# Kernel tuning notes

Measured on AMD Instinct MI355X. Metric: run time of the kernel, lower is better.

The kernel has to match this reference:

```python
import jax, jax.numpy as jnp
import numpy as np

N, E, F = 20000, 160000, 128
H, C1, C2 = 4, 128, 256
G, NCLS = 64, 10


def setup_inputs() -> dict:
    key = jax.random.key(0)
    ks = jax.random.split(key, 14)
    s = 0.05
    inp = {
        "x": jax.random.normal(ks[0], (N, F), jnp.float32),
        "edge_index": jax.random.randint(ks[1], (2, E), 0, N, dtype=jnp.int32),
        "batch": ((jnp.arange(N, dtype=jnp.int32) * G) // N),  # sorted graph ids, all 64 graphs non-empty
        # GATConv 1: in=128 -> 128 per head, heads=4, concat -> 512
        "W1": jax.random.normal(ks[2], (F, H * C1), jnp.float32) * s,
        "att_src1": jax.random.normal(ks[3], (H, C1), jnp.float32) * s,
        "att_dst1": jax.random.normal(ks[4], (H, C1), jnp.float32) * s,
        "b1": jnp.zeros((H * C1,), jnp.float32),
        # GATConv 2: in=512 -> 256, heads=1, concat=False
        "W2": jax.random.normal(ks[5], (H * C1, C2), jnp.float32) * s,
        "att_src2": jax.random.normal(ks[6], (1, C2), jnp.float32) * s,
        "att_dst2": jax.random.normal(ks[7], (1, C2), jnp.float32) * s,
        "b2": jnp.zeros((C2,), jnp.float32),
        # fc head
        "fc1_w": jax.random.normal(ks[8], (C2, 64), jnp.float32) * s,
        "fc1_b": jnp.zeros((64,), jnp.float32),
        "fc2_w": jax.random.normal(ks[9], (64, NCLS), jnp.float32) * s,
        "fc2_b": jnp.zeros((NCLS,), jnp.float32),
    }
    return inp


def gat_conv(x, src, dst, W, att_src, att_dst, bias, concat):
    """PyG GATConv: per-edge attention + segment softmax over dst + scatter-add."""
    n = x.shape[0]
    h_, c_ = att_src.shape
    h = (x @ W).reshape(n, h_, c_)                    # [N,H,C]
    a_src = jnp.einsum('nhc,hc->nh', h, att_src)       # [N,H]
    a_dst = jnp.einsum('nhc,hc->nh', h, att_dst)       # [N,H]
    e = jax.nn.leaky_relu(a_src[src] + a_dst[dst], negative_slope=0.2)  # [Etot,H]
    e_max = jax.ops.segment_max(e, dst, num_segments=n)
    ee = jnp.exp(e - e_max[dst])
    denom = jax.ops.segment_sum(ee, dst, num_segments=n)
    alpha = ee / denom[dst]                            # [Etot,H]
    out = jax.ops.segment_sum(h[src] * alpha[:, :, None], dst, num_segments=n)  # [N,H,C]
    out = out.reshape(n, h_ * c_) if concat else out.mean(axis=1)
    return out + bias


def reference(x, edge_index, batch, W1, att_src1, att_dst1, b1,
              W2, att_src2, att_dst2, b2, fc1_w, fc1_b, fc2_w, fc2_b):
    n = x.shape[0]
    # to_undirected: both directions; plus self-loops (GATConv add_self_loops=True)
    loops = jnp.arange(n, dtype=edge_index.dtype)
    src = jnp.concatenate([edge_index[0], edge_index[1], loops])
    dst = jnp.concatenate([edge_index[1], edge_index[0], loops])
    h = gat_conv(x, src, dst, W1, att_src1, att_dst1, b1, concat=True)
    h = jax.nn.relu(h)
    h = gat_conv(h, src, dst, W2, att_src2, att_dst2, b2, concat=False)
    g = jax.ops.segment_max(h, batch, num_segments=G)  # global_max_pool
    g = jax.nn.relu(g @ fc1_w + fc1_b) @ fc2_w + fc2_b
    return jax.nn.log_softmax(g, axis=1)
```

## Files before the change

### kernel.cpp

```cpp
#include <hip/hip_runtime.h>
#include <math.h>

#define FDIM 128
#define HEADS 4
#define C1DIM 128
#define C2DIM 256
#define NGRAPH 64
#define NCLS 10
#define DEGCAP 64
#define LOG2E 1.44269504088896340736f

typedef __attribute__((ext_vector_type(8))) short short8;
typedef __attribute__((ext_vector_type(4))) float float4v;
typedef __attribute__((ext_vector_type(2))) float floatx2;

__device__ __forceinline__ unsigned short f2bf(float f) {
    unsigned u = __builtin_bit_cast(unsigned, f);
    unsigned r = (u + 0x7FFFu + ((u >> 16) & 1u)) >> 16;
    return (unsigned short)r;
}
__device__ __forceinline__ float lrelu(float x) { return x > 0.f ? x : 0.2f * x; }
__device__ __forceinline__ float sel4(float a, float b, float c, float d, int hd) {
    return hd == 0 ? a : hd == 1 ? b : hd == 2 ? c : d;
}
__device__ __forceinline__ float wexp2(float x) { return __builtin_amdgcn_exp2f(lrelu(x)); }
__device__ __forceinline__ unsigned char f2fp8(float f) {
    return (unsigned char)(__builtin_amdgcn_cvt_pk_fp8_f32(f, f, 0, false) & 0xff);
}
__device__ __forceinline__ void fp8x8_dec2(int2 r, floatx2* p) {
    p[0] = __builtin_amdgcn_cvt_pk_f32_fp8(r.x, false);
    p[1] = __builtin_amdgcn_cvt_pk_f32_fp8(r.x, true);
    p[2] = __builtin_amdgcn_cvt_pk_f32_fp8(r.y, false);
    p[3] = __builtin_amdgcn_cvt_pk_f32_fp8(r.y, true);
}
__device__ __forceinline__ void fp8x4_dec2(int r, floatx2* p) {
    p[0] = __builtin_amdgcn_cvt_pk_f32_fp8(r, false);
    p[1] = __builtin_amdgcn_cvt_pk_f32_fp8(r, true);
}
__device__ __forceinline__ unsigned encf(float v) {
    unsigned b = __builtin_bit_cast(unsigned, v);
    return (b & 0x80000000u) ? ~b : (b | 0x80000000u);
}
__device__ __forceinline__ float decf(unsigned u) {
    unsigned b = (u & 0x80000000u) ? (u ^ 0x80000000u) : ~u;
    return __builtin_bit_cast(float, b);
}

__global__ __launch_bounds__(256) void prep_kernel(
        int* __restrict__ zero_base, int nzero_words,
        const float* __restrict__ x, unsigned short* __restrict__ xb, int n4,
        const float* __restrict__ W1, unsigned short* __restrict__ W1t,
        const float* __restrict__ W2, unsigned short* __restrict__ W2t,
        int ZB, int CB) {
    __shared__ float tile[32][33];
    int blk = blockIdx.x;
    if (blk < ZB) {
        int i = blk * 256 + threadIdx.x;
        if (i < nzero_words) zero_base[i] = 0;
        return;
    }
    blk -= ZB;
    if (blk < CB) {
        int i = blk * 256 + threadIdx.x;
        if (i < n4) {
            float4 v = ((const float4*)x)[i];
            ushort4 o;
            o.x = f2bf(v.x); o.y = f2bf(v.y); o.z = f2bf(v.z); o.w = f2bf(v.w);
            ((ushort4*)xb)[i] = o;
        }
        return;
    }
    blk -= CB;
    const float* W; unsigned short* Wt; int K, Nc, bx, by;
    if (blk < 64) {
        W = W1; Wt = W1t; K = 128; Nc = 512;
        bx = (blk & 15) * 32; by = (blk >> 4) * 32;
    } else {
        blk -= 64;
        W = W2; Wt = W2t; K = 512; Nc = 256;
        bx = (blk & 7) * 32; by = (blk >> 3) * 32;
    }
    int tx = threadIdx.x & 31, ty = threadIdx.x >> 5;
    #pragma unroll
    for (int r = 0; r < 32; r += 8)
        tile[ty + r][tx] = W[(size_t)(by + ty + r) * Nc + bx + tx];
    __syncthreads();
    #pragma unroll
    for (int r = 0; r < 32; r += 8)
        Wt[(size_t)(bx + ty + r) * K + by + tx] = f2bf(tile[tx][ty + r]);
}

template<int MODE>
__global__ __launch_bounds__(256) void bgemm_kernel(
        const unsigned short* __restrict__ A,
        const unsigned short* __restrict__ Bt,
        unsigned char* __restrict__ Cout,
        const float* __restrict__ att_src,
        const float* __restrict__ att_dst,
        float* __restrict__ as_out,
        float* __restrict__ ad_out,
        int M, int N_, int K,
        const int* __restrict__ ei, int E,
        int* __restrict__ cnt, int* __restrict__ esrc, int SB) {
    if (MODE == 1 && blockIdx.x < SB) {
        int i = blockIdx.x * 256 + threadIdx.x;
        if (i < 2 * E) {
            int src = ei[i];
            int dst = (i < E) ? ei[E + i] : ei[i - E];
            int pos = atomicAdd(&cnt[dst], 1);
            if (pos < DEGCAP) esrc[(dst << 6) + pos] = src;
        }
        return;
    }
    constexpr int BN = (MODE == 1) ? 128 : 256;
    constexpr int JW = BN / 32;
    constexpr int CPADB = BN + 16;
    constexpr int SMEMB = 4096 + BN * 64;
    __shared__ __align__(16) unsigned char smem[SMEMB];
    unsigned short* As = (unsigned short*)smem;
    unsigned short* Bs = (unsigned short*)(smem + 4096);
    __shared__ float sd_s[4][32];
    __shared__ float sd_d[4][32];
    const int t = threadIdx.x;
    const int lane = t & 63;
    const int wave = t >> 6;
    int row0, col0, headi;
    if (MODE == 1) {
        int bb = blockIdx.x - SB;
        headi = bb & 3;
        col0 = headi * BN;
        row0 = (bb >> 2) * 64;
    } else {
        headi = 0;
        col0 = 0;
        row0 = blockIdx.x * 64;
    }
    const int wr = (wave >> 1) * 32, wc = (wave & 1) * (BN / 2);
    float4v acc[2][JW] = {};
    for (int k0 = 0; k0 < K; k0 += 32) {
        {
            int i = t;
            int gr = row0 + (i >> 2); if (gr >= M) gr = M - 1;
            const unsigned short* gp = A + (size_t)gr * K + k0 + ((i & 3) << 3);
            __builtin_amdgcn_global_load_lds(
                (const __attribute__((address_space(1))) unsigned int*)gp,
                (__attribute__((address_space(3))) unsigned int*)&As[i * 8], 16, 0, 0);
        }
        #pragma unroll
        for (int c = 0; c < BN / 64; ++c) {
            int i = c * 256 + t;
            int gn = col0 + (i >> 2);
            const unsigned short* gp = Bt + (size_t)gn * K + k0 + ((i & 3) << 3);
            __builtin_amdgcn_global_load_lds(
                (const __attribute__((address_space(1))) unsigned int*)gp,
                (__attribute__((address_space(3))) unsigned int*)&Bs[i * 8], 16, 0, 0);
        }
        __syncthreads();
        short8 af[2], bfr[JW];
        #pragma unroll
        for (int i = 0; i < 2; ++i)
            af[i] = *(const short8*)&As[(wr + i * 16 + (lane & 15)) * 32 + (lane >> 4) * 8];
        #pragma unroll
        for (int j = 0; j < JW; ++j)
            bfr[j] = *(const short8*)&Bs[(wc + j * 16 + (lane & 15)) * 32 + (lane >> 4) * 8];
        #pragma unroll
        for (int i = 0; i < 2; ++i)
            #pragma unroll
            for (int j = 0; j < JW; ++j)
                acc[i][j] = __builtin_amdgcn_mfma_f32_16x16x32_bf16(af[i], bfr[j], acc[i][j], 0, 0, 0);
        __syncthreads();
    }
    float asv[JW], adv[JW];
    #pragma unroll
    for (int j = 0; j < JW; ++j) {
        int cc = col0 + wc + j * 16 + (lane & 15);
        asv[j] = att_src[cc];
        adv[j] = att_dst[cc];
    }
    #pragma unroll
    for (int i = 0; i < 2; ++i) {
        #pragma unroll
        for (int p = 0; p < 4; ++p) {
            int rr = wr + i * 16 + (lane >> 4) * 4 + p;
            float s = 0.f, d = 0.f;
            #pragma unroll
            for (int j = 0; j < JW; ++j) {
                smem[rr * CPADB + wc + j * 16 + (lane & 15)] = f2fp8(acc[i][j][p]);
                s += acc[i][j][p] * asv[j];
                d += acc[i][j][p] * adv[j];
            }
            #pragma unroll
            for (int o = 1; o <= 8; o <<= 1) { s += __shfl_xor(s, o); d += __shfl_xor(d, o); }
            if ((lane & 15) == 0) {
                int ridx = i * 16 + (lane >> 4) * 4 + p;
                sd_s[wave][ridx] = s;
                sd_d[wave][ridx] = d;
            }
        }
    }
    __syncthreads();
    #pragma unroll
    for (int it = 0; it < BN / 64; ++it) {
        int idx = it * 256 + t;
        int row = idx / (BN / 16), c16 = (idx % (BN / 16)) * 16;
        int grw = row0 + row;
        if (grw < M)
            *(int4*)&Cout[(size_t)grw * N_ + col0 + c16] = *(const int4*)&smem[row * CPADB + c16];
    }
    if ((wave & 1) == 0 && lane < 32) {
        float s = (sd_s[wave][lane] + sd_s[wave + 1][lane]) * LOG2E;
        float d = (sd_d[wave][lane] + sd_d[wave + 1][lane]) * LOG2E;
        int r = row0 + wr + lane;
        if (r < M) {
            if (MODE == 1) {
                as_out[r * 4 + headi] = s;
                ad_out[r * 4 + headi] = d;
            } else {
                as_out[r] = s;
                ad_out[r] = d;
            }
        }
    }
}

__global__ __launch_bounds__(256) void edge_agg1_kernel(
        const unsigned char* __restrict__ h1f8,
        const float4* __restrict__ as14,
        const float4* __restrict__ ad14,
        const int* __restrict__ cnt,
        const int* __restrict__ esrc,
        const float* __restrict__ b1,
        unsigned short* __restrict__ ho1b, int N) {
    __shared__ int sl_s[4][64];
    __shared__ __align__(16) float4 w_s[4][64];
    int wave = threadIdx.x >> 6, lane = threadIdx.x & 63;
    int node = blockIdx.x * 4 + wave;
    if (node >= N) return;
    int deg = cnt[node]; if (deg > DEGCAP) deg = DEGCAP;
    int ebase = node << 6;
    float4 asn = as14[node], adn = ad14[node];
    float w0 = wexp2(asn.x + adn.x);
    float w1 = wexp2(asn.y + adn.y);
    float w2 = wexp2(asn.z + adn.z);
    float w3 = wexp2(asn.w + adn.w);
    int hd = lane >> 4;
    unsigned c0 = (unsigned)lane * 8;
    float wsh = sel4(w0, w1, w2, w3, hd);
    floatx2 acc2[4];
    {
        int2 rs = *(const int2*)(h1f8 + ((unsigned)node << 9) + c0);
        floatx2 ds[4]; fp8x8_dec2(rs, ds);
        #pragma unroll
        for (int k = 0; k < 4; ++k) acc2[k] = wsh * ds[k];
    }
    float d0 = 0.f, d1 = 0.f, d2 = 0.f, d3 = 0.f;
    for (int cb = 0; cb < deg; cb += 64) {
        int idx = cb + lane;
        int sl = esrc[ebase + (idx < deg ? idx : deg - 1)];
        float4 wl = make_float4(0.f, 0.f, 0.f, 0.f);
        if (idx < deg) {
            float4 a = as14[sl];
            wl.x = wexp2(a.x + adn.x);
            wl.y = wexp2(a.y + adn.y);
            wl.z = wexp2(a.z + adn.z);
            wl.w = wexp2(a.w + adn.w);
            d0 += wl.x; d1 += wl.y; d2 += wl.z; d3 += wl.w;
        }
        sl_s[wave][lane] = sl << 9;
        w_s[wave][lane] = wl;
        int jmax = deg - cb; if (jmax > 64) jmax = 64;
        int j = 0;
        for (; j + 8 <= jmax; j += 8) {
            unsigned o[8]; float u[8];
            #pragma unroll
            for (int q = 0; q < 8; ++q) {
                o[q] = (unsigned)sl_s[wave][j + q] + c0;
                u[q] = ((const float*)&w_s[wave][j + q])[hd];
            }
            int2 r[8];
            #pragma unroll
            for (int q = 0; q < 8; ++q) r[q] = *(const int2*)(h1f8 + o[q]);
            #pragma unroll
            for (int q = 0; q < 8; ++q) {
                floatx2 f[4]; fp8x8_dec2(r[q], f);
                #pragma unroll
                for (int k = 0; k < 4; ++k) acc2[k] += u[q] * f[k];
            }
        }
        for (; j < jmax; ++j) {
            unsigned o0 = (unsigned)sl_s[wave][j] + c0;
            float u = ((const float*)&w_s[wave][j])[hd];
            int2 r = *(const int2*)(h1f8 + o0);
            floatx2 f[4]; fp8x8_dec2(r, f);
            #pragma unroll
            for (int k = 0; k < 4; ++k) acc2[k] += u * f[k];
        }
    }
    #pragma unroll
    for (int o = 32; o > 0; o >>= 1) {
        d0 += __shfl_xor(d0, o); d1 += __shfl_xor(d1, o);
        d2 += __shfl_xor(d2, o); d3 += __shfl_xor(d3, o);
    }
    d0 += w0; d1 += w1; d2 += w2; d3 += w3;
    float dh = sel4(d0, d1, d2, d3, hd);
    float inv = 1.f / dh;
    float4 bA = *(const float4*)&b1[c0], bB = *(const float4*)&b1[c0 + 4];
    float v0 = fmaxf(acc2[0].x * inv + bA.x, 0.f), v1 = fmaxf(acc2[0].y * inv + bA.y, 0.f);
    float v2 = fmaxf(acc2[1].x * inv + bA.z, 0.f), v3 = fmaxf(acc2[1].y * inv + bA.w, 0.f);
    float v4 = fmaxf(acc2[2].x * inv + bB.x, 0.f), v5 = fmaxf(acc2[2].y * inv + bB.y, 0.f);
    float v6 = fmaxf(acc2[3].x * inv + bB.z, 0.f), v7 = fmaxf(acc2[3].y * inv + bB.w, 0.f);
    int4 o;
    o.x = (int)((unsigned)f2bf(v0) | ((unsigned)f2bf(v1) << 16));
    o.y = (int)((unsigned)f2bf(v2) | ((unsigned)f2bf(v3) << 16));
    o.z = (int)((unsigned)f2bf(v4) | ((unsigned)f2bf(v5) << 16));
    o.w = (int)((unsigned)f2bf(v6) | ((unsigned)f2bf(v7) << 16));
    *(int4*)&ho1b[(size_t)node * 512 + c0] = o;
}

__global__ __launch_bounds__(256) void edge_agg2_kernel(
        const unsigned char* __restrict__ h2f8,
        const float* __restrict__ as2,
        const float* __restrict__ ad2,
        const int* __restrict__ cnt,
        const int* __restrict__ esrc,
        const float* __restrict__ b2,
        const int* __restrict__ batch,
        unsigned* __restrict__ pool, int N) {
    __shared__ unsigned pms[4][256];
    __shared__ int sl_s[4][64];
    __shared__ float w_s[4][64];
    int wave = threadIdx.x >> 6, lane = threadIdx.x & 63;
    int node = blockIdx.x * 4 + wave;
    bool valid = node < N;
    unsigned c0 = (unsigned)lane * 4;
    unsigned e0 = 0, e1 = 0, e2 = 0, e3 = 0;
    if (valid) {
        int deg = cnt[node]; if (deg > DEGCAP) deg = DEGCAP;
        int ebase = node << 6;
        float adn = ad2[node];
        float wself = wexp2(as2[node] + adn);
        floatx2 acc2[2];
        {
            int r = *(const int*)(h2f8 + ((unsigned)node << 8) + c0);
            floatx2 ds[2]; fp8x4_dec2(r, ds);
            acc2[0] = wself * ds[0];
            acc2[1] = wself * ds[1];
        }
        float dsum = 0.f;
        for (int cb = 0; cb < deg; cb += 64) {
            int idx = cb + lane;
            int sl = esrc[ebase + (idx < deg ? idx : deg - 1)];
            float wl = 0.f;
            if (idx < deg) {
                wl = wexp2(as2[sl] + adn);
                dsum += wl;
            }
            sl_s[wave][lane] = sl << 8;
            w_s[wave][lane] = wl;
            int jmax = deg - cb; if (jmax > 64) jmax = 64;
            int j = 0;
            for (; j + 8 <= jmax; j += 8) {
                unsigned oo[8]; float u[8]; int r[8];
                #pragma unroll
                for (int q = 0; q < 8; ++q) {
                    oo[q] = (unsigned)sl_s[wave][j + q] + c0;
                    u[q] = w_s[wave][j + q];
                }
                #pragma unroll
                for (int q = 0; q < 8; ++q) r[q] = *(const int*)(h2f8 + oo[q]);
                #pragma unroll
                for (int q = 0; q < 8; ++q) {
                    floatx2 f[2]; fp8x4_dec2(r[q], f);
                    acc2[0] += u[q] * f[0];
                    acc2[1] += u[q] * f[1];
                }
            }
            for (; j < jmax; ++j) {
                unsigned o0 = (unsigned)sl_s[wave][j] + c0;
                float u = w_s[wave][j];
                int r = *(const int*)(h2f8 + o0);
                floatx2 f[2]; fp8x4_dec2(r, f);
                acc2[0] += u * f[0];
                acc2[1] += u * f[1];
            }
        }
        #pragma unroll
        for (int o = 32; o > 0; o >>= 1) dsum += __shfl_xor(dsum, o);
        dsum += wself;
        float inv = 1.f / dsum;
        float4 bv = *(const float4*)&b2[c0];
        e0 = encf(acc2[0].x * inv + bv.x);
        e1 = encf(acc2[0].y * inv + bv.y);
        e2 = encf(acc2[1].x * inv + bv.z);
        e3 = encf(acc2[1].y * inv + bv.w);
    }
    pms[wave][c0]     = e0;
    pms[wave][c0 + 1] = e1;
    pms[wave][c0 + 2] = e2;
    pms[wave][c0 + 3] = e3;
    __syncthreads();
    int n0 = blockIdx.x * 4;
    int n3 = n0 + 3; if (n3 >= N) n3 = N - 1;
    int g0 = batch[n0], g3 = batch[n3];
    if (g0 == g3) {
        int tt = threadIdx.x;
        unsigned m0 = pms[0][tt] > pms[1][tt] ? pms[0][tt] : pms[1][tt];
        unsigned m1 = pms[2][tt] > pms[3][tt] ? pms[2][tt] : pms[3][tt];
        unsigned m = m0 > m1 ? m0 : m1;
        atomicMax(&pool[(size_t)g0 * 256 + tt], m);
    } else if (valid) {
        int g = batch[node];
        atomicMax(&pool[(size_t)g * 256 + c0], e0);
        atomicMax(&pool[(size_t)g * 256 + c0 + 1], e1);
        atomicMax(&pool[(size_t)g * 256 + c0 + 2], e2);
        atomicMax(&pool[(size_t)g * 256 + c0 + 3], e3);
    }
}

__global__ __launch_bounds__(64) void head_kernel(const unsigned* __restrict__ pool,
                                                  const float* __restrict__ fc1w,
                                                  const float* __restrict__ fc1b,
                                                  const float* __restrict__ fc2w,
                                                  const float* __restrict__ fc2b,
                                                  float* __restrict__ out) {
    __shared__ float gr[256];
    __shared__ float hid[64];
    __shared__ float o10[NCLS];
    int g = blockIdx.x, t = threadIdx.x;
    for (int i = t; i < 256; i += 64)
        gr[i] = decf(pool[(size_t)g * 256 + i]);
    __syncthreads();
    float s = fc1b[t];
    for (int k = 0; k < 256; ++k) s += gr[k] * fc1w[k * 64 + t];
    hid[t] = s > 0.f ? s : 0.f;
    __syncthreads();
    if (t < NCLS) {
        float s2 = fc2b[t];
        for (int k = 0; k < 64; ++k) s2 += hid[k] * fc2w[k * NCLS + t];
        o10[t] = s2;
    }
    __syncthreads();
    if (t == 0) {
        float mx = -INFINITY;
        for (int c = 0; c < NCLS; ++c) mx = fmaxf(mx, o10[c]);
        float se = 0.f;
        for (int c = 0; c < NCLS; ++c) se += __expf(o10[c] - mx);
        float lse = mx + logf(se);
        for (int c = 0; c < NCLS; ++c) out[g * NCLS + c] = o10[c] - lse;
    }
}

extern "C" void kernel_launch(void* const* d_in, const int* in_sizes, int n_in,
                              void* d_out, int out_size, void* d_ws, size_t ws_size,
                              hipStream_t stream) {
    (void)n_in; (void)out_size; (void)ws_size;
    const float* x        = (const float*)d_in[0];
    const int*   ei       = (const int*)d_in[1];
    const int*   batch    = (const int*)d_in[2];
    const float* W1       = (const float*)d_in[3];
    const float* att_src1 = (const float*)d_in[4];
    const float* att_dst1 = (const float*)d_in[5];
    const float* b1       = (const float*)d_in[6];
    const float* W2       = (const float*)d_in[7];
    const float* att_src2 = (const float*)d_in[8];
    const float* att_dst2 = (const float*)d_in[9];
    const float* b2       = (const float*)d_in[10];
    const float* fc1w     = (const float*)d_in[11];
    const float* fc1b     = (const float*)d_in[12];
    const float* fc2w     = (const float*)d_in[13];
    const float* fc2b     = (const float*)d_in[14];

    const int N = in_sizes[2];
    const int E = in_sizes[1] / 2;
    const int tot = 2 * E;

    char* base = (char*)d_ws;
    size_t off = 0;
    auto alloc = [&](size_t bytes) -> void* {
        void* p = base + off;
        off = (off + bytes + 255) & ~(size_t)255;
        return p;
    };
    int*      cnt    = (int*)alloc((size_t)N * 4);
    unsigned* pool   = (unsigned*)alloc((size_t)NGRAPH * 256 * 4);
    size_t zend = off;
    int*   esrc   = (int*)alloc((size_t)N * DEGCAP * 4);
    float* as1    = (float*)alloc((size_t)N * HEADS * 4);
    float* ad1    = (float*)alloc((size_t)N * HEADS * 4);
    float* as2    = (float*)alloc((size_t)N * 4);
    float* ad2    = (float*)alloc((size_t)N * 4);
    unsigned short* xb   = (unsigned short*)alloc((size_t)N * FDIM * 2);
    unsigned short* W1t  = (unsigned short*)alloc((size_t)512 * 128 * 2);
    unsigned short* W2t  = (unsigned short*)alloc((size_t)256 * 512 * 2);
    unsigned char*  h1f8 = (unsigned char*)alloc((size_t)N * 512);
    unsigned short* ho1b = (unsigned short*)alloc((size_t)N * 512 * 2);
    unsigned char*  h2f8 = (unsigned char*)alloc((size_t)N * 256);

    int nzero = (int)((zend - (size_t)((char*)cnt - base)) / 4);
    int ZB = (nzero + 255) / 256;
    int n4 = N * FDIM / 4;
    int CB = (n4 + 255) / 256;
    prep_kernel<<<ZB + CB + 64 + 128, 256, 0, stream>>>(
        cnt, nzero, x, xb, n4, W1, W1t, W2, W2t, ZB, CB);

    int SB = (tot + 255) / 256;
    int rowb = (N + 63) / 64;
    bgemm_kernel<1><<<SB + 4 * rowb, 256, 0, stream>>>(
        xb, W1t, h1f8, att_src1, att_dst1, as1, ad1, N, 512, 128, ei, E, cnt, esrc, SB);

    edge_agg1_kernel<<<(N + 3) / 4, 256, 0, stream>>>(h1f8, (const float4*)as1, (const float4*)ad1,
                                                      cnt, esrc, b1, ho1b, N);

    bgemm_kernel<2><<<rowb, 256, 0, stream>>>(
        ho1b, W2t, h2f8, att_src2, att_dst2, as2, ad2, N, 256, 512,
        nullptr, 0, nullptr, nullptr, 0);

    edge_agg2_kernel<<<(N + 3) / 4, 256, 0, stream>>>(h2f8, as2, ad2, cnt, esrc, b2,
                                                      batch, pool, N);

    head_kernel<<<NGRAPH, 64, 0, stream>>>(pool, fc1w, fc1b, fc2w, fc2b, (float*)d_out);
}
```

Measured before the change: 188.1 us.

## Split each node's edge aggregation across two waves with LDS reduction

Both edge aggregation kernels now assign two waves per destination node. Each wave handles alternate neighbours (even or odd), and the partial accumulators and softmax denominators are combined through shared memory after a block barrier. The goal is to halve the serial gather chain per wave and raise memory-level parallelism for the fp8 neighbour loads. In exchange it doubles the block count, adds barriers and LDS traffic, and leaves half the waves idle during the epilogue. The pooling step now handles pairs of nodes per block.

```diff
diff --git a/kernel.cpp b/kernel.cpp
--- a/kernel.cpp
+++ b/kernel.cpp
@@ -231,46 +231,51 @@
         const int* __restrict__ esrc,
         const float* __restrict__ b1,
         unsigned short* __restrict__ ho1b, int N) {
-    __shared__ int sl_s[4][64];
-    __shared__ __align__(16) float4 w_s[4][64];
+    __shared__ int sl_s[4][32];
+    __shared__ __align__(16) float4 w_s[4][32];
+    __shared__ float dsum_s[2][2][4];
+    __shared__ __align__(16) float accbuf[2][64][8];
     int wave = threadIdx.x >> 6, lane = threadIdx.x & 63;
-    int node = blockIdx.x * 4 + wave;
-    if (node >= N) return;
-    int deg = cnt[node]; if (deg > DEGCAP) deg = DEGCAP;
-    int ebase = node << 6;
-    float4 asn = as14[node], adn = ad14[node];
-    float w0 = wexp2(asn.x + adn.x);
-    float w1 = wexp2(asn.y + adn.y);
-    float w2 = wexp2(asn.z + adn.z);
-    float w3 = wexp2(asn.w + adn.w);
+    int nib = wave >> 1, half = wave & 1;
+    int node = blockIdx.x * 2 + nib;
+    bool valid = node < N;
     int hd = lane >> 4;
     unsigned c0 = (unsigned)lane * 8;
-    float wsh = sel4(w0, w1, w2, w3, hd);
-    floatx2 acc2[4];
-    {
-        int2 rs = *(const int2*)(h1f8 + ((unsigned)node << 9) + c0);
-        floatx2 ds[4]; fp8x8_dec2(rs, ds);
-        #pragma unroll
-        for (int k = 0; k < 4; ++k) acc2[k] = wsh * ds[k];
-    }
+    floatx2 acc2[4] = {};
     float d0 = 0.f, d1 = 0.f, d2 = 0.f, d3 = 0.f;
-    for (int cb = 0; cb < deg; cb += 64) {
-        int idx = cb + lane;
-        int sl = esrc[ebase + (idx < deg ? idx : deg - 1)];
-        float4 wl = make_float4(0.f, 0.f, 0.f, 0.f);
-        if (idx < deg) {
+    float ws0 = 0.f, ws1 = 0.f, ws2 = 0.f, ws3 = 0.f;
+    int nh = 0;
+    if (valid) {
+        int deg = cnt[node]; if (deg > DEGCAP) deg = DEGCAP;
+        int ebase = node << 6;
+        float4 adn = ad14[node];
+        nh = (deg + 1 - half) >> 1;
+        if (lane < nh) {
+            int sl = esrc[ebase + half + 2 * lane];
             float4 a = as14[sl];
+            float4 wl;
             wl.x = wexp2(a.x + adn.x);
             wl.y = wexp2(a.y + adn.y);
             wl.z = wexp2(a.z + adn.z);
             wl.w = wexp2(a.w + adn.w);
-            d0 += wl.x; d1 += wl.y; d2 += wl.z; d3 += wl.w;
-        }
-        sl_s[wave][lane] = sl << 9;
-        w_s[wave][lane] = wl;
-        int jmax = deg - cb; if (jmax > 64) jmax = 64;
+            d0 = wl.x; d1 = wl.y; d2 = wl.z; d3 = wl.w;
+            sl_s[wave][lane] = sl << 9;
+            w_s[wave][lane] = wl;
+        }
+        if (half == 0) {
+            float4 asn = as14[node];
+            ws0 = wexp2(asn.x + adn.x);
+            ws1 = wexp2(asn.y + adn.y);
+            ws2 = wexp2(asn.z + adn.z);
+            ws3 = wexp2(asn.w + adn.w);
+            float wsh = sel4(ws0, ws1, ws2, ws3, hd);
+            int2 rs = *(const int2*)(h1f8 + ((unsigned)node << 9) + c0);
+            floatx2 ds[4]; fp8x8_dec2(rs, ds);
+            #pragma unroll
+            for (int k = 0; k < 4; ++k) acc2[k] = wsh * ds[k];
+        }
         int j = 0;
-        for (; j + 8 <= jmax; j += 8) {
+        for (; j + 8 <= nh; j += 8) {
             unsigned o[8]; float u[8];
             #pragma unroll
             for (int q = 0; q < 8; ++q) {
@@ -287,7 +292,7 @@
                 for (int k = 0; k < 4; ++k) acc2[k] += u[q] * f[k];
             }
         }
-        for (; j < jmax; ++j) {
+        for (; j < nh; ++j) {
             unsigned o0 = (unsigned)sl_s[wave][j] + c0;
             float u = ((const float*)&w_s[wave][j])[hd];
             int2 r = *(const int2*)(h1f8 + o0);
@@ -301,20 +306,35 @@
         d0 += __shfl_xor(d0, o); d1 += __shfl_xor(d1, o);
         d2 += __shfl_xor(d2, o); d3 += __shfl_xor(d3, o);
     }
-    d0 += w0; d1 += w1; d2 += w2; d3 += w3;
-    float dh = sel4(d0, d1, d2, d3, hd);
-    float inv = 1.f / dh;
-    float4 bA = *(const float4*)&b1[c0], bB = *(const float4*)&b1[c0 + 4];
-    float v0 = fmaxf(acc2[0].x * inv + bA.x, 0.f), v1 = fmaxf(acc2[0].y * inv + bA.y, 0.f);
-    float v2 = fmaxf(acc2[1].x * inv + bA.z, 0.f), v3 = fmaxf(acc2[1].y * inv + bA.w, 0.f);
-    float v4 = fmaxf(acc2[2].x * inv + bB.x, 0.f), v5 = fmaxf(acc2[2].y * inv + bB.y, 0.f);
-    float v6 = fmaxf(acc2[3].x * inv + bB.z, 0.f), v7 = fmaxf(acc2[3].y * inv + bB.w, 0.f);
-    int4 o;
-    o.x = (int)((unsigned)f2bf(v0) | ((unsigned)f2bf(v1) << 16));
-    o.y = (int)((unsigned)f2bf(v2) | ((unsigned)f2bf(v3) << 16));
-    o.z = (int)((unsigned)f2bf(v4) | ((unsigned)f2bf(v5) << 16));
-    o.w = (int)((unsigned)f2bf(v6) | ((unsigned)f2bf(v7) << 16));
-    *(int4*)&ho1b[(size_t)node * 512 + c0] = o;
+    if (half == 0) { d0 += ws0; d1 += ws1; d2 += ws2; d3 += ws3; }
+    if (lane == 0) {
+        dsum_s[nib][half][0] = d0; dsum_s[nib][half][1] = d1;
+        dsum_s[nib][half][2] = d2; dsum_s[nib][half][3] = d3;
+    }
+    if (half == 1) {
+        *(float4*)&accbuf[nib][lane][0] = make_float4(acc2[0].x, acc2[0].y, acc2[1].x, acc2[1].y);
+        *(float4*)&accbuf[nib][lane][4] = make_float4(acc2[2].x, acc2[2].y, acc2[3].x, acc2[3].y);
+    }
+    __syncthreads();
+    if (valid && half == 0) {
+        float4 A0 = *(const float4*)&accbuf[nib][lane][0];
+        float4 A1 = *(const float4*)&accbuf[nib][lane][4];
+        acc2[0].x += A0.x; acc2[0].y += A0.y; acc2[1].x += A0.z; acc2[1].y += A0.w;
+        acc2[2].x += A1.x; acc2[2].y += A1.y; acc2[3].x += A1.z; acc2[3].y += A1.w;
+        float dh = dsum_s[nib][0][hd] + dsum_s[nib][1][hd];
+        float inv = 1.f / dh;
+        float4 bA = *(const float4*)&b1[c0], bB = *(const float4*)&b1[c0 + 4];
+        float v0 = fmaxf(acc2[0].x * inv + bA.x, 0.f), v1 = fmaxf(acc2[0].y * inv + bA.y, 0.f);
+        float v2 = fmaxf(acc2[1].x * inv + bA.z, 0.f), v3 = fmaxf(acc2[1].y * inv + bA.w, 0.f);
+        float v4 = fmaxf(acc2[2].x * inv + bB.x, 0.f), v5 = fmaxf(acc2[2].y * inv + bB.y, 0.f);
+        float v6 = fmaxf(acc2[3].x * inv + bB.z, 0.f), v7 = fmaxf(acc2[3].y * inv + bB.w, 0.f);
+        int4 o;
+        o.x = (int)((unsigned)f2bf(v0) | ((unsigned)f2bf(v1) << 16));
+        o.y = (int)((unsigned)f2bf(v2) | ((unsigned)f2bf(v3) << 16));
+        o.z = (int)((unsigned)f2bf(v4) | ((unsigned)f2bf(v5) << 16));
+        o.w = (int)((unsigned)f2bf(v6) | ((unsigned)f2bf(v7) << 16));
+        *(int4*)&ho1b[(size_t)node * 512 + c0] = o;
+    }
 }
 
 __global__ __launch_bounds__(256) void edge_agg2_kernel(
@@ -326,94 +346,100 @@
         const float* __restrict__ b2,
         const int* __restrict__ batch,
         unsigned* __restrict__ pool, int N) {
-    __shared__ unsigned pms[4][256];
-    __shared__ int sl_s[4][64];
-    __shared__ float w_s[4][64];
+    __shared__ unsigned pms[2][256];
+    __shared__ int sl_s[4][32];
+    __shared__ float w_s[4][32];
+    __shared__ float dsum_s[2][2];
+    __shared__ __align__(16) float accbuf[2][64][4];
     int wave = threadIdx.x >> 6, lane = threadIdx.x & 63;
-    int node = blockIdx.x * 4 + wave;
+    int nib = wave >> 1, half = wave & 1;
+    int node = blockIdx.x * 2 + nib;
     bool valid = node < N;
     unsigned c0 = (unsigned)lane * 4;
-    unsigned e0 = 0, e1 = 0, e2 = 0, e3 = 0;
+    floatx2 acc2[2] = {};
+    float dsum = 0.f, wself = 0.f;
+    int nh = 0;
     if (valid) {
         int deg = cnt[node]; if (deg > DEGCAP) deg = DEGCAP;
         int ebase = node << 6;
         float adn = ad2[node];
-        float wself = wexp2(as2[node] + adn);
-        floatx2 acc2[2];
-        {
+        nh = (deg + 1 - half) >> 1;
+        if (lane < nh) {
+            int sl = esrc[ebase + half + 2 * lane];
+            float wl = wexp2(as2[sl] + adn);
+            dsum = wl;
+            sl_s[wave][lane] = sl << 8;
+            w_s[wave][lane] = wl;
+        }
+        if (half == 0) {
+            wself = wexp2(as2[node] + adn);
             int r = *(const int*)(h2f8 + ((unsigned)node << 8) + c0);
             floatx2 ds[2]; fp8x4_dec2(r, ds);
             acc2[0] = wself * ds[0];
             acc2[1] = wself * ds[1];
         }
-        float dsum = 0.f;
-        for (int cb = 0; cb < deg; cb += 64) {
-            int idx = cb + lane;
-            int sl = esrc[ebase + (idx < deg ? idx : deg - 1)];
-            float wl = 0.f;
-            if (idx < deg) {
-                wl = wexp2(as2[sl] + adn);
-                dsum += wl;
-            }
-            sl_s[wave][lane] = sl << 8;
-            w_s[wave][lane] = wl;
-            int jmax = deg - cb; if (jmax > 64) jmax = 64;
-            int j = 0;
-            for (; j + 8 <= jmax; j += 8) {
-                unsigned oo[8]; float u[8]; int r[8];
-                #pragma unroll
-                for (int q = 0; q < 8; ++q) {
-                    oo[q] = (unsigned)sl_s[wave][j + q] + c0;
-                    u[q] = w_s[wave][j + q];
-                }
-                #pragma unroll
-                for (int q = 0; q < 8; ++q) r[q] = *(const int*)(h2f8 + oo[q]);
-                #pragma unroll
-                for (int q = 0; q < 8; ++q) {
-                    floatx2 f[2]; fp8x4_dec2(r[q], f);
-                    acc2[0] += u[q] * f[0];
-                    acc2[1] += u[q] * f[1];
-                }
-            }
-            for (; j < jmax; ++j) {
-                unsigned o0 = (unsigned)sl_s[wave][j] + c0;
-                float u = w_s[wave][j];
-                int r = *(const int*)(h2f8 + o0);
-                floatx2 f[2]; fp8x4_dec2(r, f);
-                acc2[0] += u * f[0];
-                acc2[1] += u * f[1];
-            }
-        }
-        #pragma unroll
-        for (int o = 32; o > 0; o >>= 1) dsum += __shfl_xor(dsum, o);
-        dsum += wself;
-        float inv = 1.f / dsum;
-        float4 bv = *(const float4*)&b2[c0];
-        e0 = encf(acc2[0].x * inv + bv.x);
-        e1 = encf(acc2[0].y * inv + bv.y);
-        e2 = encf(acc2[1].x * inv + bv.z);
-        e3 = encf(acc2[1].y * inv + bv.w);
-    }
-    pms[wave][c0]     = e0;
-    pms[wave][c0 + 1] = e1;
-    pms[wave][c0 + 2] = e2;
-    pms[wave][c0 + 3] = e3;
-    __syncthreads();
-    int n0 = blockIdx.x * 4;
-    int n3 = n0 + 3; if (n3 >= N) n3 = N - 1;
-    int g0 = batch[n0], g3 = batch[n3];
-    if (g0 == g3) {
-        int tt = threadIdx.x;
-        unsigned m0 = pms[0][tt] > pms[1][tt] ? pms[0][tt] : pms[1][tt];
-        unsigned m1 = pms[2][tt] > pms[3][tt] ? pms[2][tt] : pms[3][tt];
-        unsigned m = m0 > m1 ? m0 : m1;
+        int j = 0;
+        for (; j + 8 <= nh; j += 8) {
+            unsigned oo[8]; float u[8]; int r[8];
+            #pragma unroll
+            for (int q = 0; q < 8; ++q) {
+                oo[q] = (unsigned)sl_s[wave][j + q] + c0;
+                u[q] = w_s[wave][j + q];
+            }
+            #pragma unroll
+            for (int q = 0; q < 8; ++q) r[q] = *(const int*)(h2f8 + oo[q]);
+            #pragma unroll
+            for (int q = 0; q < 8; ++q) {
+                floatx2 f[2]; fp8x4_dec2(r[q], f);
+                acc2[0] += u[q] * f[0];
+                acc2[1] += u[q] * f[1];
+            }
+        }
+        for (; j < nh; ++j) {
+            unsigned o0 = (unsigned)sl_s[wave][j] + c0;
+            float u = w_s[wave][j];
+            int r = *(const int*)(h2f8 + o0);
+            floatx2 f[2]; fp8x4_dec2(r, f);
+            acc2[0] += u * f[0];
+            acc2[1] += u * f[1];
+        }
+    }
+    #pragma unroll
+    for (int o = 32; o > 0; o >>= 1) dsum += __shfl_xor(dsum, o);
+    if (half == 0) dsum += wself;
+    if (lane == 0) dsum_s[nib][half] = dsum;
+    if (half == 1)
+        *(float4*)&accbuf[nib][lane][0] = make_float4(acc2[0].x, acc2[0].y, acc2[1].x, acc2[1].y);
+    __syncthreads();
+    if (half == 0) {
+        unsigned e0 = 0, e1 = 0, e2 = 0, e3 = 0;
+        if (valid) {
+            float4 A0 = *(const float4*)&accbuf[nib][lane][0];
+            acc2[0].x += A0.x; acc2[0].y += A0.y; acc2[1].x += A0.z; acc2[1].y += A0.w;
+            float dh = dsum_s[nib][0] + dsum_s[nib][1];
+            float inv = 1.f / dh;
+            float4 bv = *(const float4*)&b2[c0];
+            e0 = encf(acc2[0].x * inv + bv.x);
+            e1 = encf(acc2[0].y * inv + bv.y);
+            e2 = encf(acc2[1].x * inv + bv.z);
+            e3 = encf(acc2[1].y * inv + bv.w);
+        }
+        pms[nib][c0]     = e0;
+        pms[nib][c0 + 1] = e1;
+        pms[nib][c0 + 2] = e2;
+        pms[nib][c0 + 3] = e3;
+    }
+    __syncthreads();
+    int n0 = blockIdx.x * 2;
+    int n1 = n0 + 1; if (n1 >= N) n1 = N - 1;
+    int g0 = batch[n0], g1 = batch[n1];
+    int tt = threadIdx.x;
+    if (g0 == g1) {
+        unsigned m = pms[0][tt] > pms[1][tt] ? pms[0][tt] : pms[1][tt];
         atomicMax(&pool[(size_t)g0 * 256 + tt], m);
-    } else if (valid) {
-        int g = batch[node];
-        atomicMax(&pool[(size_t)g * 256 + c0], e0);
-        atomicMax(&pool[(size_t)g * 256 + c0 + 1], e1);
-        atomicMax(&pool[(size_t)g * 256 + c0 + 2], e2);
-        atomicMax(&pool[(size_t)g * 256 + c0 + 3], e3);
+    } else {
+        atomicMax(&pool[(size_t)g0 * 256 + tt], pms[0][tt]);
+        atomicMax(&pool[(size_t)g1 * 256 + tt], pms[1][tt]);
     }
 }
 
@@ -508,14 +534,14 @@
     bgemm_kernel<1><<<SB + 4 * rowb, 256, 0, stream>>>(
         xb, W1t, h1f8, att_src1, att_dst1, as1, ad1, N, 512, 128, ei, E, cnt, esrc, SB);
 
-    edge_agg1_kernel<<<(N + 3) / 4, 256, 0, stream>>>(h1f8, (const float4*)as1, (const float4*)ad1,
+    edge_agg1_kernel<<<(N + 1) / 2, 256, 0, stream>>>(h1f8, (const float4*)as1, (const float4*)ad1,
                                                       cnt, esrc, b1, ho1b, N);
 
     bgemm_kernel<2><<<rowb, 256, 0, stream>>>(
         ho1b, W2t, h2f8, att_src2, att_dst2, as2, ad2, N, 256, 512,
         nullptr, 0, nullptr, nullptr, 0);
 
-    edge_agg2_kernel<<<(N + 3) / 4, 256, 0, stream>>>(h2f8, as2, ad2, cnt, esrc, b2,
+    edge_agg2_kernel<<<(N + 1) / 2, 256, 0, stream>>>(h2f8, as2, ad2, cnt, esrc, b2,
                                                       batch, pool, N);
 
     head_kernel<<<NGRAPH, 64, 0, stream>>>(pool, fc1w, fc1b, fc2w, fc2b, (float*)d_out);
```

Result: slower. 214.8 us (+14.2%).

## Split layer-1 edge aggregation per head across blocks and use nontemporal gathers

Applied to the files above, without the earlier changes.

The layer-1 aggregation kernel now launches four times as many blocks, with each block handling one attention head for four nodes. Inside a wave, 16 lanes cover the head's 128 channels and four edge slots run in parallel, with a cross-lane shuffle reduction at the end. This is meant to raise parallelism and spread the gathers over more waves. Feature gathers in both aggregation kernels now use nontemporal loads to avoid polluting the cache. In exchange, edge indices and weights are reloaded once per head, extra shuffle reductions are added, and the new edge_agg1 assumes degree ≤ 64, which holds under DEGCAP.

```diff
diff --git a/kernel.cpp b/kernel.cpp
--- a/kernel.cpp
+++ b/kernel.cpp
@@ -20,12 +20,13 @@
     return (unsigned short)r;
 }
 __device__ __forceinline__ float lrelu(float x) { return x > 0.f ? x : 0.2f * x; }
-__device__ __forceinline__ float sel4(float a, float b, float c, float d, int hd) {
-    return hd == 0 ? a : hd == 1 ? b : hd == 2 ? c : d;
-}
 __device__ __forceinline__ float wexp2(float x) { return __builtin_amdgcn_exp2f(lrelu(x)); }
 __device__ __forceinline__ unsigned char f2fp8(float f) {
     return (unsigned char)(__builtin_amdgcn_cvt_pk_fp8_f32(f, f, 0, false) & 0xff);
+}
+__device__ __forceinline__ int2 nt_load8(const unsigned char* p) {
+    long long v = __builtin_nontemporal_load((const long long*)p);
+    return __builtin_bit_cast(int2, v);
 }
 __device__ __forceinline__ void fp8x8_dec2(int2 r, floatx2* p) {
     p[0] = __builtin_amdgcn_cvt_pk_f32_fp8(r.x, false);
@@ -225,96 +226,71 @@
 
 __global__ __launch_bounds__(256) void edge_agg1_kernel(
         const unsigned char* __restrict__ h1f8,
-        const float4* __restrict__ as14,
-        const float4* __restrict__ ad14,
+        const float* __restrict__ as1,
+        const float* __restrict__ ad1,
         const int* __restrict__ cnt,
         const int* __restrict__ esrc,
         const float* __restrict__ b1,
         unsigned short* __restrict__ ho1b, int N) {
     __shared__ int sl_s[4][64];
-    __shared__ __align__(16) float4 w_s[4][64];
+    __shared__ float w_s[4][64];
     int wave = threadIdx.x >> 6, lane = threadIdx.x & 63;
-    int node = blockIdx.x * 4 + wave;
+    int s = blockIdx.x & 3;
+    int node = (blockIdx.x >> 2) * 4 + wave;
     if (node >= N) return;
     int deg = cnt[node]; if (deg > DEGCAP) deg = DEGCAP;
-    int ebase = node << 6;
-    float4 asn = as14[node], adn = ad14[node];
-    float w0 = wexp2(asn.x + adn.x);
-    float w1 = wexp2(asn.y + adn.y);
-    float w2 = wexp2(asn.z + adn.z);
-    float w3 = wexp2(asn.w + adn.w);
-    int hd = lane >> 4;
-    unsigned c0 = (unsigned)lane * 8;
-    float wsh = sel4(w0, w1, w2, w3, hd);
-    floatx2 acc2[4];
-    {
-        int2 rs = *(const int2*)(h1f8 + ((unsigned)node << 9) + c0);
-        floatx2 ds[4]; fp8x8_dec2(rs, ds);
-        #pragma unroll
-        for (int k = 0; k < 4; ++k) acc2[k] = wsh * ds[k];
-    }
-    float d0 = 0.f, d1 = 0.f, d2 = 0.f, d3 = 0.f;
-    for (int cb = 0; cb < deg; cb += 64) {
-        int idx = cb + lane;
-        int sl = esrc[ebase + (idx < deg ? idx : deg - 1)];
-        float4 wl = make_float4(0.f, 0.f, 0.f, 0.f);
-        if (idx < deg) {
-            float4 a = as14[sl];
-            wl.x = wexp2(a.x + adn.x);
-            wl.y = wexp2(a.y + adn.y);
-            wl.z = wexp2(a.z + adn.z);
-            wl.w = wexp2(a.w + adn.w);
-            d0 += wl.x; d1 += wl.y; d2 += wl.z; d3 += wl.w;
-        }
-        sl_s[wave][lane] = sl << 9;
-        w_s[wave][lane] = wl;
-        int jmax = deg - cb; if (jmax > 64) jmax = 64;
-        int j = 0;
-        for (; j + 8 <= jmax; j += 8) {
-            unsigned o[8]; float u[8];
-            #pragma unroll
-            for (int q = 0; q < 8; ++q) {
-                o[q] = (unsigned)sl_s[wave][j + q] + c0;
-                u[q] = ((const float*)&w_s[wave][j + q])[hd];
-            }
-            int2 r[8];
-            #pragma unroll
-            for (int q = 0; q < 8; ++q) r[q] = *(const int2*)(h1f8 + o[q]);
-            #pragma unroll
-            for (int q = 0; q < 8; ++q) {
-                floatx2 f[4]; fp8x8_dec2(r[q], f);
-                #pragma unroll
-                for (int k = 0; k < 4; ++k) acc2[k] += u[q] * f[k];
-            }
-        }
-        for (; j < jmax; ++j) {
-            unsigned o0 = (unsigned)sl_s[wave][j] + c0;
-            float u = ((const float*)&w_s[wave][j])[hd];
-            int2 r = *(const int2*)(h1f8 + o0);
-            floatx2 f[4]; fp8x8_dec2(r, f);
-            #pragma unroll
-            for (int k = 0; k < 4; ++k) acc2[k] += u * f[k];
-        }
-    }
-    #pragma unroll
-    for (int o = 32; o > 0; o >>= 1) {
-        d0 += __shfl_xor(d0, o); d1 += __shfl_xor(d1, o);
-        d2 += __shfl_xor(d2, o); d3 += __shfl_xor(d3, o);
-    }
-    d0 += w0; d1 += w1; d2 += w2; d3 += w3;
-    float dh = sel4(d0, d1, d2, d3, hd);
-    float inv = 1.f / dh;
-    float4 bA = *(const float4*)&b1[c0], bB = *(const float4*)&b1[c0 + 4];
-    float v0 = fmaxf(acc2[0].x * inv + bA.x, 0.f), v1 = fmaxf(acc2[0].y * inv + bA.y, 0.f);
-    float v2 = fmaxf(acc2[1].x * inv + bA.z, 0.f), v3 = fmaxf(acc2[1].y * inv + bA.w, 0.f);
-    float v4 = fmaxf(acc2[2].x * inv + bB.x, 0.f), v5 = fmaxf(acc2[2].y * inv + bB.y, 0.f);
-    float v6 = fmaxf(acc2[3].x * inv + bB.z, 0.f), v7 = fmaxf(acc2[3].y * inv + bB.w, 0.f);
-    int4 o;
-    o.x = (int)((unsigned)f2bf(v0) | ((unsigned)f2bf(v1) << 16));
-    o.y = (int)((unsigned)f2bf(v2) | ((unsigned)f2bf(v3) << 16));
-    o.z = (int)((unsigned)f2bf(v4) | ((unsigned)f2bf(v5) << 16));
-    o.w = (int)((unsigned)f2bf(v6) | ((unsigned)f2bf(v7) << 16));
-    *(int4*)&ho1b[(size_t)node * 512 + c0] = o;
+    unsigned cb = (unsigned)s << 7;
+    int cw = lane & 15, es = lane >> 4;
+    float adn = ad1[node * 4 + s];
+    float wself = wexp2(as1[node * 4 + s] + adn);
+    float w = 0.f;
+    if (lane < deg) {
+        int sl = esrc[(node << 6) + lane];
+        w = wexp2(as1[sl * 4 + s] + adn);
+        sl_s[wave][lane] = (sl << 9) + (int)cb;
+        w_s[wave][lane] = w;
+    }
+    float dsum = w;
+    #pragma unroll
+    for (int o = 32; o > 0; o >>= 1) dsum += __shfl_xor(dsum, o);
+    dsum += wself;
+    floatx2 acc2[4] = {};
+    if (es == 0) {
+        int2 r = nt_load8(h1f8 + ((unsigned)node << 9) + cb + cw * 8);
+        floatx2 f[4]; fp8x8_dec2(r, f);
+        #pragma unroll
+        for (int k = 0; k < 4; ++k) acc2[k] = wself * f[k];
+    }
+    #pragma unroll 2
+    for (int j = 0; j < deg; j += 4) {
+        int e = j + es;
+        unsigned o0 = (unsigned)sl_s[wave][e < deg ? e : 0] + cw * 8;
+        float u = e < deg ? w_s[wave][e] : 0.f;
+        int2 r = nt_load8(h1f8 + o0);
+        floatx2 f[4]; fp8x8_dec2(r, f);
+        #pragma unroll
+        for (int k = 0; k < 4; ++k) acc2[k] += u * f[k];
+    }
+    #pragma unroll
+    for (int k = 0; k < 4; ++k) {
+        acc2[k].x += __shfl_xor(acc2[k].x, 16); acc2[k].x += __shfl_xor(acc2[k].x, 32);
+        acc2[k].y += __shfl_xor(acc2[k].y, 16); acc2[k].y += __shfl_xor(acc2[k].y, 32);
+    }
+    if (es == 0) {
+        float inv = 1.f / dsum;
+        int ch0 = (int)cb + cw * 8;
+        float4 bA = *(const float4*)&b1[ch0], bB = *(const float4*)&b1[ch0 + 4];
+        float v0 = fmaxf(acc2[0].x * inv + bA.x, 0.f), v1 = fmaxf(acc2[0].y * inv + bA.y, 0.f);
+        float v2 = fmaxf(acc2[1].x * inv + bA.z, 0.f), v3 = fmaxf(acc2[1].y * inv + bA.w, 0.f);
+        float v4 = fmaxf(acc2[2].x * inv + bB.x, 0.f), v5 = fmaxf(acc2[2].y * inv + bB.y, 0.f);
+        float v6 = fmaxf(acc2[3].x * inv + bB.z, 0.f), v7 = fmaxf(acc2[3].y * inv + bB.w, 0.f);
+        int4 o;
+        o.x = (int)((unsigned)f2bf(v0) | ((unsigned)f2bf(v1) << 16));
+        o.y = (int)((unsigned)f2bf(v2) | ((unsigned)f2bf(v3) << 16));
+        o.z = (int)((unsigned)f2bf(v4) | ((unsigned)f2bf(v5) << 16));
+        o.w = (int)((unsigned)f2bf(v6) | ((unsigned)f2bf(v7) << 16));
+        *(int4*)&ho1b[(size_t)node * 512 + ch0] = o;
+    }
 }
 
 __global__ __launch_bounds__(256) void edge_agg2_kernel(
@@ -341,7 +317,8 @@
         float wself = wexp2(as2[node] + adn);
         floatx2 acc2[2];
         {
-            int r = *(const int*)(h2f8 + ((unsigned)node << 8) + c0);
+            int r = __builtin_nontemporal_load(
+                (const int*)(h2f8 + ((unsigned)node << 8) + c0));
             floatx2 ds[2]; fp8x4_dec2(r, ds);
             acc2[0] = wself * ds[0];
             acc2[1] = wself * ds[1];
@@ -367,7 +344,8 @@
                     u[q] = w_s[wave][j + q];
                 }
                 #pragma unroll
-                for (int q = 0; q < 8; ++q) r[q] = *(const int*)(h2f8 + oo[q]);
+                for (int q = 0; q < 8; ++q)
+                    r[q] = __builtin_nontemporal_load((const int*)(h2f8 + oo[q]));
                 #pragma unroll
                 for (int q = 0; q < 8; ++q) {
                     floatx2 f[2]; fp8x4_dec2(r[q], f);
@@ -378,7 +356,7 @@
             for (; j < jmax; ++j) {
                 unsigned o0 = (unsigned)sl_s[wave][j] + c0;
                 float u = w_s[wave][j];
-                int r = *(const int*)(h2f8 + o0);
+                int r = __builtin_nontemporal_load((const int*)(h2f8 + o0));
                 floatx2 f[2]; fp8x4_dec2(r, f);
                 acc2[0] += u * f[0];
                 acc2[1] += u * f[1];
@@ -508,8 +486,8 @@
     bgemm_kernel<1><<<SB + 4 * rowb, 256, 0, stream>>>(
         xb, W1t, h1f8, att_src1, att_dst1, as1, ad1, N, 512, 128, ei, E, cnt, esrc, SB);
 
-    edge_agg1_kernel<<<(N + 3) / 4, 256, 0, stream>>>(h1f8, (const float4*)as1, (const float4*)ad1,
-                                                      cnt, esrc, b1, ho1b, N);
+    edge_agg1_kernel<<<((N + 3) / 4) * 4, 256, 0, stream>>>(h1f8, as1, ad1,
+                                                            cnt, esrc, b1, ho1b, N);
 
     bgemm_kernel<2><<<rowb, 256, 0, stream>>>(
         ho1b, W2t, h2f8, att_src2, att_dst2, as2, ad2, N, 256, 512,
```

Result: slower. 222.2 us (+18.1%).
